# Kernel optimization log

Measured on AMD Instinct MI355X. Metric: run time of the kernel, lower is better.

## Reference

```python
import jax, jax.numpy as jnp
import numpy as np

B, L, D, H, NL, V, W = 4, 2048, 512, 8, 4, 258, 8
HD = D // H


def setup_inputs() -> dict:
    key = jax.random.key(0)
    ks = jax.random.split(key, 12)
    s = 0.02
    x = jax.random.randint(ks[0], (B, L), 0, V, dtype=jnp.int32)
    patch_lengths = jnp.full((B, 256), W, dtype=jnp.int32)  # sum over patches == L
    emb = jax.random.normal(ks[1], (V, D), jnp.float32) * s
    ent_w = jax.random.normal(ks[2], (D, 1), jnp.float32) * s
    ent_b = jnp.zeros((D,), jnp.float32)
    qkv_w = jax.random.normal(ks[3], (NL, 3 * D, D), jnp.float32) * s
    qkv_b = jnp.zeros((NL, 3 * D), jnp.float32)
    ao_w = jax.random.normal(ks[4], (NL, D, D), jnp.float32) * s
    ao_b = jnp.zeros((NL, D), jnp.float32)
    ln1_s = jnp.ones((NL, D), jnp.float32)
    ln1_b = jnp.zeros((NL, D), jnp.float32)
    ln2_s = jnp.ones((NL, D), jnp.float32)
    ln2_b = jnp.zeros((NL, D), jnp.float32)
    ff1_w = jax.random.normal(ks[5], (NL, 4 * D, D), jnp.float32) * s
    ff1_b = jnp.zeros((NL, 4 * D), jnp.float32)
    ff2_w = jax.random.normal(ks[6], (NL, D, 4 * D), jnp.float32) * s
    ff2_b = jnp.zeros((NL, D), jnp.float32)
    out_w = jax.random.normal(ks[7], (V, D), jnp.float32) * s
    return {"emb": emb, "ent_w": ent_w, "ent_b": ent_b, "qkv_w": qkv_w,
            "qkv_b": qkv_b, "ao_w": ao_w, "ao_b": ao_b, "ln1_s": ln1_s,
            "ln1_b": ln1_b, "ln2_s": ln2_s, "ln2_b": ln2_b, "ff1_w": ff1_w,
            "ff1_b": ff1_b, "ff2_w": ff2_w, "ff2_b": ff2_b, "out_w": out_w,
            "x": x, "patch_lengths": patch_lengths}


def _layernorm(h, scale, bias, eps=1e-5):
    mu = jnp.mean(h, axis=-1, keepdims=True)
    var = jnp.mean(jnp.square(h - mu), axis=-1, keepdims=True)
    return (h - mu) * jax.lax.rsqrt(var + eps) * scale + bias


def _entropy_features(x, dtype):
    # fused sliding-window histogram via one-hot cumsum (replaces per-window bincount loop)
    onehot = jax.nn.one_hot(x, 256, dtype=dtype)            # [B, L, 256]
    c = jnp.cumsum(onehot, axis=1)
    cpad = jnp.concatenate([jnp.zeros_like(c[:, :1]), c], axis=1)
    counts = cpad[:, W:] - cpad[:, :-W]                     # [B, L-W+1, 256]
    p = counts / W
    ent = -jnp.sum(p * jnp.log2(p + 1e-10), axis=-1)        # zero-count terms contribute exactly 0
    full = jnp.zeros(x.shape, dtype).at[:, :x.shape[1] - W + 1].set(ent)
    return full[..., None]                                  # [B, L, 1]


def _block(h, p):
    qkv_w, qkv_b, ao_w, ao_b, l1s, l1b, l2s, l2b, f1w, f1b, f2w, f2b = p
    g = _layernorm(h, l1s, l1b)
    qkv = g @ qkv_w.T + qkv_b                                # [B, L, 3D]
    q, k, v = jnp.split(qkv, 3, axis=-1)
    q = q.reshape(B, L, H, HD)
    k = k.reshape(B, L, H, HD)
    v = v.reshape(B, L, H, HD)
    scores = jnp.einsum('blhd,bmhd->bhlm', q, k) / np.sqrt(HD).astype(h.dtype)
    attn = jax.nn.softmax(scores, axis=-1)
    o = jnp.einsum('bhlm,bmhd->blhd', attn, v).reshape(B, L, D)
    h = h + o @ ao_w.T + ao_b
    g = _layernorm(h, l2s, l2b)
    g = jax.nn.gelu(g @ f1w.T + f1b, approximate=False) @ f2w.T + f2b
    return h + g, None


def reference(emb, ent_w, ent_b, qkv_w, qkv_b, ao_w, ao_b, ln1_s, ln1_b,
              ln2_s, ln2_b, ff1_w, ff1_b, ff2_w, ff2_b, out_w, x, patch_lengths):
    tok = emb[x]                                             # [B, L, D]
    ent = _entropy_features(x, tok.dtype)                    # [B, L, 1]
    ent_emb = ent * ent_w[:, 0] + ent_b                      # Linear(1, D)
    h = tok + ent_emb
    h, _ = jax.lax.scan(_block, h,
                        (qkv_w, qkv_b, ao_w, ao_b, ln1_s, ln1_b,
                         ln2_s, ln2_b, ff1_w, ff1_b, ff2_w, ff2_b))
    # NOTE: the original module's global_transformer/patch-pool branch does not
    # feed the returned logits (dead code); logits come from the local stream h.
    logits = h @ out_w.T                                     # [B, L, V]
    return logits
```

## Files before the change

kernel.cpp:

```cpp
#include <hip/hip_runtime.h>
#include <hip/hip_bf16.h>
#include <math.h>

#define BB 4
#define LL 2048
#define DD 512
#define HH 8
#define NLAYER 4
#define VV 258
#define WW 8
#define HDIM 64
#define MM (BB * LL)
#define VPAD 384

typedef __attribute__((ext_vector_type(8))) short short8v;
typedef __attribute__((ext_vector_type(4))) float float4v;

typedef __attribute__((address_space(3))) unsigned int lds_u32;
typedef const __attribute__((address_space(1))) unsigned int glb_u32;

__device__ __forceinline__ unsigned short f2bf(float x) {
    unsigned int u = __float_as_uint(x);
    unsigned int r = (u + 0x7fffu + ((u >> 16) & 1u)) >> 16;
    return (unsigned short)r;
}

__device__ __forceinline__ unsigned lds_addr(const void* p) {
    return (unsigned)(size_t)(__attribute__((address_space(3))) const void*)p;
}

__global__ __launch_bounds__(256)
void cvt_kernel(const float* __restrict__ in, unsigned short* __restrict__ out, int n)
{
    int i = (blockIdx.x * 256 + threadIdx.x) * 4;
    if (i < n) {
        float4 v = *reinterpret_cast<const float4*>(in + i);
        uint2 pk;
        pk.x = (unsigned)f2bf(v.x) | ((unsigned)f2bf(v.y) << 16);
        pk.y = (unsigned)f2bf(v.z) | ((unsigned)f2bf(v.w) << 16);
        *reinterpret_cast<uint2*>(out + i) = pk;
    }
}

__global__ __launch_bounds__(256)
void cvt_pad_kernel(const float* __restrict__ in, unsigned short* __restrict__ out)
{
    int i = blockIdx.x * 256 + threadIdx.x;
    int row = i >> 9;
    out[i] = (row < VV) ? f2bf(in[i]) : (unsigned short)0;
}

__global__ __launch_bounds__(256)
void embed_ln_kernel(const int* __restrict__ x,
                     const float* __restrict__ emb,
                     const float* __restrict__ ent_w,
                     const float* __restrict__ ent_b,
                     const float* __restrict__ ln_s,
                     const float* __restrict__ ln_b,
                     float* __restrict__ h,
                     unsigned short* __restrict__ g)
{
    int w = threadIdx.x >> 6, lane = threadIdx.x & 63;
    int row = blockIdx.x * 4 + w;
    int b = row / LL, l = row % LL;

    float ent = 0.f;
    if (l <= LL - WW) {
        int win[WW];
        #pragma unroll
        for (int i = 0; i < WW; i++) win[i] = x[b * LL + l + i];
        float s = 0.f;
        #pragma unroll
        for (int i = 0; i < WW; i++) {
            if (win[i] < 256) {
                int c = 0;
                #pragma unroll
                for (int j = 0; j < WW; j++) c += (win[j] == win[i]) ? 1 : 0;
                s += log2f((float)c * 0.125f + 1e-10f);
            }
        }
        ent = -s * 0.125f;
    }

    int tok = x[row];
    const float* erow = emb + (size_t)tok * DD + lane * 8;
    float v[8], ew[8], eb[8];
    *reinterpret_cast<float4*>(v)      = *reinterpret_cast<const float4*>(erow);
    *reinterpret_cast<float4*>(v + 4)  = *reinterpret_cast<const float4*>(erow + 4);
    *reinterpret_cast<float4*>(ew)     = *reinterpret_cast<const float4*>(ent_w + lane * 8);
    *reinterpret_cast<float4*>(ew + 4) = *reinterpret_cast<const float4*>(ent_w + lane * 8 + 4);
    *reinterpret_cast<float4*>(eb)     = *reinterpret_cast<const float4*>(ent_b + lane * 8);
    *reinterpret_cast<float4*>(eb + 4) = *reinterpret_cast<const float4*>(ent_b + lane * 8 + 4);

    float sum = 0.f, sq = 0.f;
    #pragma unroll
    for (int i = 0; i < 8; i++) {
        v[i] = v[i] + ent * ew[i] + eb[i];
        sum += v[i]; sq += v[i] * v[i];
    }
    float* hr = h + (size_t)row * DD + lane * 8;
    *reinterpret_cast<float4*>(hr)     = *reinterpret_cast<const float4*>(v);
    *reinterpret_cast<float4*>(hr + 4) = *reinterpret_cast<const float4*>(v + 4);

    #pragma unroll
    for (int off = 32; off > 0; off >>= 1) {
        sum += __shfl_xor(sum, off);
        sq  += __shfl_xor(sq, off);
    }
    float mu = sum * (1.f / DD);
    float var = sq * (1.f / DD) - mu * mu;
    float rstd = rsqrtf(var + 1e-5f);

    float s8[8], bi[8];
    *reinterpret_cast<float4*>(s8)     = *reinterpret_cast<const float4*>(ln_s + lane * 8);
    *reinterpret_cast<float4*>(s8 + 4) = *reinterpret_cast<const float4*>(ln_s + lane * 8 + 4);
    *reinterpret_cast<float4*>(bi)     = *reinterpret_cast<const float4*>(ln_b + lane * 8);
    *reinterpret_cast<float4*>(bi + 4) = *reinterpret_cast<const float4*>(ln_b + lane * 8 + 4);

    unsigned int pk[4];
    #pragma unroll
    for (int i = 0; i < 4; i++) {
        unsigned short lo = f2bf((v[2*i]   - mu) * rstd * s8[2*i]   + bi[2*i]);
        unsigned short hi = f2bf((v[2*i+1] - mu) * rstd * s8[2*i+1] + bi[2*i+1]);
        pk[i] = (unsigned)lo | ((unsigned)hi << 16);
    }
    *reinterpret_cast<uint4*>(g + (size_t)row * DD + lane * 8) =
        *reinterpret_cast<const uint4*>(pk);
}

__global__ __launch_bounds__(256)
void ln_kernel(const float* __restrict__ h,
               const float* __restrict__ scale,
               const float* __restrict__ bias,
               unsigned short* __restrict__ g)
{
    int w = threadIdx.x >> 6, lane = threadIdx.x & 63;
    int row = blockIdx.x * 4 + w;
    const float* hr = h + (size_t)row * DD + lane * 8;

    float v[8];
    *reinterpret_cast<float4*>(v)     = *reinterpret_cast<const float4*>(hr);
    *reinterpret_cast<float4*>(v + 4) = *reinterpret_cast<const float4*>(hr + 4);

    float sum = 0.f, sq = 0.f;
    #pragma unroll
    for (int i = 0; i < 8; i++) { sum += v[i]; sq += v[i] * v[i]; }
    #pragma unroll
    for (int off = 32; off > 0; off >>= 1) {
        sum += __shfl_xor(sum, off);
        sq  += __shfl_xor(sq, off);
    }
    float mu = sum * (1.f / DD);
    float var = sq * (1.f / DD) - mu * mu;
    float rstd = rsqrtf(var + 1e-5f);

    float s[8], bi[8];
    *reinterpret_cast<float4*>(s)      = *reinterpret_cast<const float4*>(scale + lane * 8);
    *reinterpret_cast<float4*>(s + 4)  = *reinterpret_cast<const float4*>(scale + lane * 8 + 4);
    *reinterpret_cast<float4*>(bi)     = *reinterpret_cast<const float4*>(bias + lane * 8);
    *reinterpret_cast<float4*>(bi + 4) = *reinterpret_cast<const float4*>(bias + lane * 8 + 4);

    unsigned int pk[4];
    #pragma unroll
    for (int i = 0; i < 4; i++) {
        unsigned short lo = f2bf((v[2*i]   - mu) * rstd * s[2*i]   + bi[2*i]);
        unsigned short hi = f2bf((v[2*i+1] - mu) * rstd * s[2*i+1] + bi[2*i+1]);
        pk[i] = (unsigned)lo | ((unsigned)hi << 16);
    }
    *reinterpret_cast<uint4*>(g + (size_t)row * DD + lane * 8) =
        *reinterpret_cast<const uint4*>(pk);
}

template<bool HAS_BIAS, bool GELU, bool RESID, int OMODE>
__global__ __launch_bounds__(256)
void gemm_mfma(const unsigned short* __restrict__ A,
               const unsigned short* __restrict__ W,
               const float* __restrict__ bias,
               const float* __restrict__ resid,
               void* __restrict__ Cv,
               unsigned short* __restrict__ Cb,
               int Nn, int Kk)
{
    __shared__ unsigned short As[2][128 * 64];
    __shared__ unsigned short Bs[2][128 * 64];

    int t = threadIdx.x;
    int w = t >> 6, lane = t & 63;
    int wr = w >> 1, wc = w & 1;
    int l15 = lane & 15, l4 = lane >> 4;
    int m0 = blockIdx.y * 128, n0 = blockIdx.x * 128;

    int lrow = lane >> 3;
    int segp = (lane & 7) ^ lrow;

    float4v acc[4][4];
    #pragma unroll
    for (int i = 0; i < 4; i++)
        #pragma unroll
        for (int j = 0; j < 4; j++)
            acc[i][j] = (float4v){0.f, 0.f, 0.f, 0.f};

    #define STAGE(buf, k0) do {                                                   \
        _Pragma("unroll")                                                         \
        for (int i_ = 0; i_ < 4; i_++) {                                          \
            int r_ = i_ * 32 + w * 8 + lrow;                                      \
            __builtin_amdgcn_global_load_lds(                                     \
                (glb_u32*)(A + (size_t)(m0 + r_) * Kk + (k0) + segp * 8),         \
                (lds_u32*)(As[buf] + i_ * 2048 + w * 512), 16, 0, 0);             \
            __builtin_amdgcn_global_load_lds(                                     \
                (glb_u32*)(W + (size_t)(n0 + r_) * Kk + (k0) + segp * 8),         \
                (lds_u32*)(Bs[buf] + i_ * 2048 + w * 512), 16, 0, 0);             \
        } } while (0)

    int nk = Kk >> 6;
    STAGE(0, 0);
    for (int kt = 0; kt < nk; kt++) {
        int cur = kt & 1;
        if (kt + 1 < nk) {
            STAGE(cur ^ 1, (kt + 1) << 6);
            __builtin_amdgcn_sched_barrier(0);
            asm volatile("s_waitcnt vmcnt(8)");
            __builtin_amdgcn_sched_barrier(0);
        } else {
            __builtin_amdgcn_sched_barrier(0);
            asm volatile("s_waitcnt vmcnt(0)");
            __builtin_amdgcn_sched_barrier(0);
        }
        __builtin_amdgcn_s_barrier();

        const char* asb = (const char*)As[cur];
        const char* bsb = (const char*)Bs[cur];
        #pragma unroll
        for (int kc = 0; kc < 2; kc++) {
            short8v af[4], bfr[4];
            #pragma unroll
            for (int mf = 0; mf < 4; mf++) {
                int row = wr * 64 + mf * 16 + l15;
                int off = (row * 128 + kc * 64 + l4 * 16) ^ ((row & 7) << 4);
                af[mf] = *reinterpret_cast<const short8v*>(asb + off);
            }
            #pragma unroll
            for (int nf = 0; nf < 4; nf++) {
                int row = wc * 64 + nf * 16 + l15;
                int off = (row * 128 + kc * 64 + l4 * 16) ^ ((row & 7) << 4);
                bfr[nf] = *reinterpret_cast<const short8v*>(bsb + off);
            }
            #pragma unroll
            for (int mf = 0; mf < 4; mf++)
                #pragma unroll
                for (int nf = 0; nf < 4; nf++)
                    acc[mf][nf] = __builtin_amdgcn_mfma_f32_16x16x32_bf16(
                        af[mf], bfr[nf], acc[mf][nf], 0, 0, 0);
        }
        __builtin_amdgcn_s_barrier();
    }
    #undef STAGE

    #pragma unroll
    for (int mf = 0; mf < 4; mf++)
        #pragma unroll
        for (int nf = 0; nf < 4; nf++)
            #pragma unroll
            for (int r = 0; r < 4; r++) {
                int m = m0 + wr * 64 + mf * 16 + l4 * 4 + r;
                int n = n0 + wc * 64 + nf * 16 + l15;
                if (n < Nn) {
                    float v = acc[mf][nf][r];
                    if (HAS_BIAS) v += bias[n];
                    if (GELU)     v = 0.5f * v * (1.f + erff(v * 0.70710678118654752f));
                    if (RESID)    v += resid[(size_t)m * Nn + n];
                    if (OMODE == 1) {
                        ((unsigned short*)Cv)[(size_t)m * Nn + n] = f2bf(v);
                    } else {
                        ((float*)Cv)[(size_t)m * Nn + n] = v;
                        if (OMODE == 2) Cb[(size_t)m * Nn + n] = f2bf(v);
                    }
                }
            }
}

__global__ __launch_bounds__(512, 2)
void attn_mfma(const unsigned short* __restrict__ qkv, unsigned short* __restrict__ o)
{
    __shared__ unsigned short Kl[2][64 * 64];
    __shared__ unsigned short Vs[2][64 * 64];
    __shared__ unsigned short Pl[8 * 16 * 64];
    __shared__ float Scl[8][16];

    int t = threadIdx.x, w = t >> 6, lane = t & 63;
    int l15 = lane & 15, l4 = lane >> 4;

    int flat = blockIdx.x;
    int swz = (flat & 7) * 64 + (flat >> 3);
    int qt = swz & 15, hh = (swz >> 4) & 7, b = swz >> 7;

    int q0 = qt * 128 + w * 16;
    const int RS = 3 * DD;

    short8v qf[2];
    #pragma unroll
    for (int dh = 0; dh < 2; dh++) {
        size_t addr = (size_t)(b * LL + q0 + l15) * RS + hh * HDIM + dh * 32 + l4 * 8;
        qf[dh] = *reinterpret_cast<const short8v*>(qkv + addr);
    }

    float4v o_acc[4];
    #pragma unroll
    for (int dt = 0; dt < 4; dt++) o_acc[dt] = (float4v){0.f, 0.f, 0.f, 0.f};
    float m_run = -1e30f, l_run = 0.f;

    char* pbase = (char*)Pl + w * 2048;

    int krow = t >> 3, kseg = t & 7;
    int vrow = ((t >> 5) << 2) | ((t >> 1) & 3);
    int vseg = (((t >> 3) & 3) << 1) | (t & 1);
    int koff = (krow * 128 + kseg * 16) ^ ((krow & 7) << 4);
    int voff = t * 16;

    const unsigned short* kptr = qkv + (size_t)(b * LL + krow) * RS + hh * HDIM + DD + kseg * 8;
    const unsigned short* vptr = qkv + (size_t)(b * LL + vrow) * RS + hh * HDIM + 2 * DD + vseg * 8;
    const int step = 64 * RS;

    unsigned vtrbase = lds_addr(Vs) + ((lane >> 4) << 10)
                     + (((lane >> 2) & 3) << 5) + ((lane & 3) << 3);

    {
        short8v krg = *reinterpret_cast<const short8v*>(kptr); kptr += step;
        short8v vrg = *reinterpret_cast<const short8v*>(vptr); vptr += step;
        *reinterpret_cast<short8v*>((char*)Kl[0] + koff) = krg;
        *reinterpret_cast<short8v*>((char*)Vs[0] + voff) = vrg;
    }
    __syncthreads();

    for (int kb = 0; kb < LL / 64; kb++) {
        int cur = kb & 1;
        short8v krg, vrg;
        if (kb + 1 < LL / 64) {
            krg = *reinterpret_cast<const short8v*>(kptr); kptr += step;
            vrg = *reinterpret_cast<const short8v*>(vptr); vptr += step;
        }

        const char* klc = (const char*)Kl[cur];
        unsigned vb = vtrbase + cur * 8192;

        float4v s_acc[4];
        __builtin_amdgcn_s_setprio(1);
        #pragma unroll
        for (int nt = 0; nt < 4; nt++) {
            s_acc[nt] = (float4v){0.f, 0.f, 0.f, 0.f};
            #pragma unroll
            for (int dh = 0; dh < 2; dh++) {
                int row = nt * 16 + l15;
                int off = (row * 128 + dh * 64 + l4 * 16) ^ ((row & 7) << 4);
                short8v kf = *reinterpret_cast<const short8v*>(klc + off);
                s_acc[nt] = __builtin_amdgcn_mfma_f32_16x16x32_bf16(kf, qf[dh], s_acc[nt], 0, 0, 0);
            }
        }
        __builtin_amdgcn_s_setprio(0);

        float mm = -1e30f;
        #pragma unroll
        for (int nt = 0; nt < 4; nt++)
            #pragma unroll
            for (int r = 0; r < 4; r++)
                mm = fmaxf(mm, s_acc[nt][r]);
        mm *= 0.125f;
        mm = fmaxf(mm, __shfl_xor(mm, 16));
        mm = fmaxf(mm, __shfl_xor(mm, 32));

        if (!__all(mm <= m_run + 8.f)) {
            float mnew = fmaxf(m_run, mm);
            float sc = __expf(m_run - mnew);
            m_run = mnew;
            l_run *= sc;
            if (l4 == 0) Scl[w][l15] = sc;
            float4 scv = *reinterpret_cast<const float4*>(&Scl[w][l4 * 4]);
            #pragma unroll
            for (int dt = 0; dt < 4; dt++) {
                o_acc[dt][0] *= scv.x; o_acc[dt][1] *= scv.y;
                o_acc[dt][2] *= scv.z; o_acc[dt][3] *= scv.w;
            }
        }

        float ps = 0.f;
        #pragma unroll
        for (int nt = 0; nt < 4; nt++) {
            float p0 = __expf(fmaf(s_acc[nt][0], 0.125f, -m_run));
            float p1 = __expf(fmaf(s_acc[nt][1], 0.125f, -m_run));
            float p2 = __expf(fmaf(s_acc[nt][2], 0.125f, -m_run));
            float p3 = __expf(fmaf(s_acc[nt][3], 0.125f, -m_run));
            ps += (p0 + p1) + (p2 + p3);
            unsigned int pk0, pk1;
            asm("v_cvt_pk_bf16_f32 %0, %1, %2" : "=v"(pk0) : "v"(p0), "v"(p1));
            asm("v_cvt_pk_bf16_f32 %0, %1, %2" : "=v"(pk1) : "v"(p2), "v"(p3));
            uint2 pk; pk.x = pk0; pk.y = pk1;
            int off = (l15 * 128 + nt * 32 + l4 * 8) ^ ((l15 & 7) << 4);
            *reinterpret_cast<uint2*>(pbase + off) = pk;
        }
        l_run += ps;

        #pragma unroll
        for (int kc = 0; kc < 2; kc++) {
            int poff = (l15 * 128 + kc * 64 + l4 * 16) ^ ((l15 & 7) << 4);
            short8v pf = *reinterpret_cast<const short8v*>(pbase + poff);
            unsigned long long tr0, tr1, tr2, tr3, tr4, tr5, tr6, tr7;
            unsigned ab = vb + kc * 4096;
            asm volatile("ds_read_b64_tr_b16 %0, %1" : "=v"(tr0) : "v"(ab));
            asm volatile("ds_read_b64_tr_b16 %0, %1" : "=v"(tr1) : "v"(ab + 512));
            asm volatile("ds_read_b64_tr_b16 %0, %1" : "=v"(tr2) : "v"(ab + 128));
            asm volatile("ds_read_b64_tr_b16 %0, %1" : "=v"(tr3) : "v"(ab + 640));
            asm volatile("ds_read_b64_tr_b16 %0, %1" : "=v"(tr4) : "v"(ab + 256));
            asm volatile("ds_read_b64_tr_b16 %0, %1" : "=v"(tr5) : "v"(ab + 768));
            asm volatile("ds_read_b64_tr_b16 %0, %1" : "=v"(tr6) : "v"(ab + 384));
            asm volatile("ds_read_b64_tr_b16 %0, %1" : "=v"(tr7) : "v"(ab + 896));
            asm volatile("s_waitcnt lgkmcnt(0)");
            __builtin_amdgcn_sched_barrier(0);
            __builtin_amdgcn_s_setprio(1);
            union { unsigned long long q[2]; short8v v; } u0, u1, u2, u3;
            u0.q[0] = tr0; u0.q[1] = tr1;
            u1.q[0] = tr2; u1.q[1] = tr3;
            u2.q[0] = tr4; u2.q[1] = tr5;
            u3.q[0] = tr6; u3.q[1] = tr7;
            o_acc[0] = __builtin_amdgcn_mfma_f32_16x16x32_bf16(pf, u0.v, o_acc[0], 0, 0, 0);
            o_acc[1] = __builtin_amdgcn_mfma_f32_16x16x32_bf16(pf, u1.v, o_acc[1], 0, 0, 0);
            o_acc[2] = __builtin_amdgcn_mfma_f32_16x16x32_bf16(pf, u2.v, o_acc[2], 0, 0, 0);
            o_acc[3] = __builtin_amdgcn_mfma_f32_16x16x32_bf16(pf, u3.v, o_acc[3], 0, 0, 0);
            __builtin_amdgcn_s_setprio(0);
        }

        if (kb + 1 < LL / 64) {
            *reinterpret_cast<short8v*>((char*)Kl[cur ^ 1] + koff) = krg;
            *reinterpret_cast<short8v*>((char*)Vs[cur ^ 1] + voff) = vrg;
        }
        __syncthreads();
    }

    float lt = l_run;
    lt += __shfl_xor(lt, 16);
    lt += __shfl_xor(lt, 32);
    if (l4 == 0) Scl[w][l15] = 1.f / lt;
    float4 iv = *reinterpret_cast<const float4*>(&Scl[w][l4 * 4]);
    float invs[4] = {iv.x, iv.y, iv.z, iv.w};
    #pragma unroll
    for (int r = 0; r < 4; r++) {
        int qg = q0 + l4 * 4 + r;
        #pragma unroll
        for (int dt = 0; dt < 4; dt++) {
            o[(size_t)(b * LL + qg) * DD + hh * HDIM + dt * 16 + l15] =
                f2bf(o_acc[dt][r] * invs[r]);
        }
    }
}

extern "C" void kernel_launch(void* const* d_in, const int* in_sizes, int n_in,
                              void* d_out, int out_size, void* d_ws, size_t ws_size,
                              hipStream_t stream)
{
    const float* emb    = (const float*)d_in[0];
    const float* ent_w  = (const float*)d_in[1];
    const float* ent_b  = (const float*)d_in[2];
    const float* qkv_w  = (const float*)d_in[3];
    const float* qkv_b  = (const float*)d_in[4];
    const float* ao_w   = (const float*)d_in[5];
    const float* ao_b   = (const float*)d_in[6];
    const float* ln1_s  = (const float*)d_in[7];
    const float* ln1_b  = (const float*)d_in[8];
    const float* ln2_s  = (const float*)d_in[9];
    const float* ln2_b  = (const float*)d_in[10];
    const float* ff1_w  = (const float*)d_in[11];
    const float* ff1_b  = (const float*)d_in[12];
    const float* ff2_w  = (const float*)d_in[13];
    const float* ff2_b  = (const float*)d_in[14];
    const float* out_w  = (const float*)d_in[15];
    const int*   x      = (const int*)d_in[16];

    float* out = (float*)d_out;

    const int NQW = NLAYER * 3 * DD * DD;
    const int NAW = NLAYER * DD * DD;
    const int NF1 = NLAYER * 4 * DD * DD;
    const int NF2 = NLAYER * DD * 4 * DD;

    char* p = (char*)d_ws;
    unsigned short* wq  = (unsigned short*)p; p += (size_t)NQW * 2;
    unsigned short* wa  = (unsigned short*)p; p += (size_t)NAW * 2;
    unsigned short* w1  = (unsigned short*)p; p += (size_t)NF1 * 2;
    unsigned short* w2  = (unsigned short*)p; p += (size_t)NF2 * 2;
    unsigned short* wob = (unsigned short*)p; p += (size_t)VPAD * DD * 2;
    float*          h   = (float*)p;          p += (size_t)MM * DD * 4;
    unsigned short* hb  = (unsigned short*)p; p += (size_t)MM * DD * 2;
    unsigned short* gb  = (unsigned short*)p; p += (size_t)MM * DD * 2;
    unsigned short* ob  = (unsigned short*)p; p += (size_t)MM * DD * 2;
    unsigned short* bb  = (unsigned short*)p; p += (size_t)MM * 4 * DD * 2;

    dim3 blk(256);

    cvt_kernel<<<NQW / 1024, blk, 0, stream>>>(qkv_w, wq, NQW);
    cvt_kernel<<<NAW / 1024, blk, 0, stream>>>(ao_w,  wa, NAW);
    cvt_kernel<<<NF1 / 1024, blk, 0, stream>>>(ff1_w, w1, NF1);
    cvt_kernel<<<NF2 / 1024, blk, 0, stream>>>(ff2_w, w2, NF2);
    cvt_pad_kernel<<<(VPAD * DD) / 256, blk, 0, stream>>>(out_w, wob);

    embed_ln_kernel<<<MM / 4, blk, 0, stream>>>(x, emb, ent_w, ent_b,
                                                ln1_s, ln1_b, h, gb);

    for (int layer = 0; layer < NLAYER; layer++) {
        const unsigned short* qw = wq + (size_t)layer * 3 * DD * DD;
        const unsigned short* aw = wa + (size_t)layer * DD * DD;
        const unsigned short* f1 = w1 + (size_t)layer * 4 * DD * DD;
        const unsigned short* f2 = w2 + (size_t)layer * DD * 4 * DD;
        const float* qb  = qkv_b + (size_t)layer * 3 * DD;
        const float* ab  = ao_b  + (size_t)layer * DD;
        const float* l1s = ln1_s + (size_t)layer * DD;
        const float* l1b = ln1_b + (size_t)layer * DD;
        const float* l2s = ln2_s + (size_t)layer * DD;
        const float* l2b = ln2_b + (size_t)layer * DD;
        const float* f1b = ff1_b + (size_t)layer * 4 * DD;
        const float* f2b = ff2_b + (size_t)layer * DD;

        if (layer > 0)
            ln_kernel<<<MM / 4, blk, 0, stream>>>(h, l1s, l1b, gb);

        {
            dim3 grid((3 * DD) / 128, MM / 128);
            gemm_mfma<true, false, false, 1><<<grid, blk, 0, stream>>>(
                gb, qw, qb, nullptr, bb, nullptr, 3 * DD, DD);
        }

        attn_mfma<<<512, 512, 0, stream>>>(bb, ob);

        {
            dim3 grid(DD / 128, MM / 128);
            gemm_mfma<true, false, true, 0><<<grid, blk, 0, stream>>>(
                ob, aw, ab, h, h, nullptr, DD, DD);
        }

        ln_kernel<<<MM / 4, blk, 0, stream>>>(h, l2s, l2b, gb);

        {
            dim3 grid((4 * DD) / 128, MM / 128);
            gemm_mfma<true, true, false, 1><<<grid, blk, 0, stream>>>(
                gb, f1, f1b, nullptr, bb, nullptr, 4 * DD, DD);
        }

        {
            dim3 grid(DD / 128, MM / 128);
            if (layer == NLAYER - 1)
                gemm_mfma<true, false, true, 2><<<grid, blk, 0, stream>>>(
                    bb, f2, f2b, h, h, hb, DD, 4 * DD);
            else
                gemm_mfma<true, false, true, 0><<<grid, blk, 0, stream>>>(
                    bb, f2, f2b, h, h, nullptr, DD, 4 * DD);
        }
    }

    {
        dim3 grid(VPAD / 128, MM / 128);
        gemm_mfma<false, false, false, 0><<<grid, blk, 0, stream>>>(
            hb, wob, nullptr, nullptr, out, nullptr, VV, DD);
    }
}
```

Measured before the change: 782.2 us.

## Narrow GEMM N-tile for small-N GEMMs and restructure attention softmax/PV loads

Templates the GEMM on the N-tile width and uses 64-wide tiles for the N=512 and vocab GEMMs, doubling the block count so more CUs are occupied. In attention, switches the softmax to exp2 with the scale pre-multiplied by log2(e), and issues all P and V transposed LDS reads up front with staged waitcnts so MFMAs start while later reads are still in flight. The narrower tiles give less B-tile reuse per loaded A tile, and the hand-written waitcnt sequencing depends on the reads completing in issue order.

Result: no change. 788.1 us (+0.8%).

```diff
diff --git a/kernel.cpp b/kernel.cpp
--- a/kernel.cpp
+++ b/kernel.cpp
@@ -13,6 +13,9 @@
 #define MM (BB * LL)
 #define VPAD 384
 
+#define C8 0.18033688f
+#define THR2 11.54156f
+
 typedef __attribute__((ext_vector_type(8))) short short8v;
 typedef __attribute__((ext_vector_type(4))) float float4v;
 
@@ -171,7 +174,7 @@
         *reinterpret_cast<const uint4*>(pk);
 }
 
-template<bool HAS_BIAS, bool GELU, bool RESID, int OMODE>
+template<bool HAS_BIAS, bool GELU, bool RESID, int OMODE, int BN>
 __global__ __launch_bounds__(256)
 void gemm_mfma(const unsigned short* __restrict__ A,
                const unsigned short* __restrict__ W,
@@ -181,23 +184,24 @@
                unsigned short* __restrict__ Cb,
                int Nn, int Kk)
 {
+    constexpr int NF = BN / 32;
     __shared__ unsigned short As[2][128 * 64];
-    __shared__ unsigned short Bs[2][128 * 64];
+    __shared__ unsigned short Bs[2][BN * 64];
 
     int t = threadIdx.x;
     int w = t >> 6, lane = t & 63;
     int wr = w >> 1, wc = w & 1;
     int l15 = lane & 15, l4 = lane >> 4;
-    int m0 = blockIdx.y * 128, n0 = blockIdx.x * 128;
+    int m0 = blockIdx.y * 128, n0 = blockIdx.x * BN;
 
     int lrow = lane >> 3;
     int segp = (lane & 7) ^ lrow;
 
-    float4v acc[4][4];
+    float4v acc[4][NF];
     #pragma unroll
     for (int i = 0; i < 4; i++)
         #pragma unroll
-        for (int j = 0; j < 4; j++)
+        for (int j = 0; j < NF; j++)
             acc[i][j] = (float4v){0.f, 0.f, 0.f, 0.f};
 
     #define STAGE(buf, k0) do {                                                   \
@@ -207,6 +211,10 @@
             __builtin_amdgcn_global_load_lds(                                     \
                 (glb_u32*)(A + (size_t)(m0 + r_) * Kk + (k0) + segp * 8),         \
                 (lds_u32*)(As[buf] + i_ * 2048 + w * 512), 16, 0, 0);             \
+        }                                                                         \
+        _Pragma("unroll")                                                         \
+        for (int i_ = 0; i_ < NF; i_++) {                                         \
+            int r_ = i_ * 32 + w * 8 + lrow;                                      \
             __builtin_amdgcn_global_load_lds(                                     \
                 (glb_u32*)(W + (size_t)(n0 + r_) * Kk + (k0) + segp * 8),         \
                 (lds_u32*)(Bs[buf] + i_ * 2048 + w * 512), 16, 0, 0);             \
@@ -219,7 +227,8 @@
         if (kt + 1 < nk) {
             STAGE(cur ^ 1, (kt + 1) << 6);
             __builtin_amdgcn_sched_barrier(0);
-            asm volatile("s_waitcnt vmcnt(8)");
+            if constexpr (BN == 128) asm volatile("s_waitcnt vmcnt(8)");
+            else                     asm volatile("s_waitcnt vmcnt(6)");
             __builtin_amdgcn_sched_barrier(0);
         } else {
             __builtin_amdgcn_sched_barrier(0);
@@ -232,7 +241,7 @@
         const char* bsb = (const char*)Bs[cur];
         #pragma unroll
         for (int kc = 0; kc < 2; kc++) {
-            short8v af[4], bfr[4];
+            short8v af[4], bfr[NF];
             #pragma unroll
             for (int mf = 0; mf < 4; mf++) {
                 int row = wr * 64 + mf * 16 + l15;
@@ -240,15 +249,15 @@
                 af[mf] = *reinterpret_cast<const short8v*>(asb + off);
             }
             #pragma unroll
-            for (int nf = 0; nf < 4; nf++) {
-                int row = wc * 64 + nf * 16 + l15;
+            for (int nf = 0; nf < NF; nf++) {
+                int row = wc * (BN / 2) + nf * 16 + l15;
                 int off = (row * 128 + kc * 64 + l4 * 16) ^ ((row & 7) << 4);
                 bfr[nf] = *reinterpret_cast<const short8v*>(bsb + off);
             }
             #pragma unroll
             for (int mf = 0; mf < 4; mf++)
                 #pragma unroll
-                for (int nf = 0; nf < 4; nf++)
+                for (int nf = 0; nf < NF; nf++)
                     acc[mf][nf] = __builtin_amdgcn_mfma_f32_16x16x32_bf16(
                         af[mf], bfr[nf], acc[mf][nf], 0, 0, 0);
         }
@@ -259,11 +268,11 @@
     #pragma unroll
     for (int mf = 0; mf < 4; mf++)
         #pragma unroll
-        for (int nf = 0; nf < 4; nf++)
+        for (int nf = 0; nf < NF; nf++)
             #pragma unroll
             for (int r = 0; r < 4; r++) {
                 int m = m0 + wr * 64 + mf * 16 + l4 * 4 + r;
-                int n = n0 + wc * 64 + nf * 16 + l15;
+                int n = n0 + wc * (BN / 2) + nf * 16 + l15;
                 if (n < Nn) {
                     float v = acc[mf][nf][r];
                     if (HAS_BIAS) v += bias[n];
@@ -323,6 +332,9 @@
 
     unsigned vtrbase = lds_addr(Vs) + ((lane >> 4) << 10)
                      + (((lane >> 2) & 3) << 5) + ((lane & 3) << 3);
+    unsigned pswz = (unsigned)((l15 & 7) << 4);
+    unsigned pa0 = lds_addr(pbase) + ((unsigned)(l15 * 128 + l4 * 16) ^ pswz);
+    unsigned pa1 = lds_addr(pbase) + ((unsigned)(l15 * 128 + 64 + l4 * 16) ^ pswz);
 
     {
         short8v krg = *reinterpret_cast<const short8v*>(kptr); kptr += step;
@@ -358,19 +370,20 @@
         }
         __builtin_amdgcn_s_setprio(0);
 
-        float mm = -1e30f;
-        #pragma unroll
-        for (int nt = 0; nt < 4; nt++)
-            #pragma unroll
-            for (int r = 0; r < 4; r++)
-                mm = fmaxf(mm, s_acc[nt][r]);
-        mm *= 0.125f;
+        float t0 = fmaxf(fmaxf(s_acc[0][0], s_acc[0][1]), s_acc[0][2]);
+        float t1 = fmaxf(fmaxf(s_acc[0][3], s_acc[1][0]), s_acc[1][1]);
+        float t2 = fmaxf(fmaxf(s_acc[1][2], s_acc[1][3]), s_acc[2][0]);
+        float t3 = fmaxf(fmaxf(s_acc[2][1], s_acc[2][2]), s_acc[2][3]);
+        float t4 = fmaxf(fmaxf(s_acc[3][0], s_acc[3][1]), s_acc[3][2]);
+        float mm = fmaxf(fmaxf(fmaxf(t0, t1), t2),
+                         fmaxf(fmaxf(t3, t4), s_acc[3][3]));
+        mm *= C8;
         mm = fmaxf(mm, __shfl_xor(mm, 16));
         mm = fmaxf(mm, __shfl_xor(mm, 32));
 
-        if (!__all(mm <= m_run + 8.f)) {
+        if (!__all(mm <= m_run + THR2)) {
             float mnew = fmaxf(m_run, mm);
-            float sc = __expf(m_run - mnew);
+            float sc = __builtin_amdgcn_exp2f(m_run - mnew);
             m_run = mnew;
             l_run *= sc;
             if (l4 == 0) Scl[w][l15] = sc;
@@ -385,10 +398,10 @@
         float ps = 0.f;
         #pragma unroll
         for (int nt = 0; nt < 4; nt++) {
-            float p0 = __expf(fmaf(s_acc[nt][0], 0.125f, -m_run));
-            float p1 = __expf(fmaf(s_acc[nt][1], 0.125f, -m_run));
-            float p2 = __expf(fmaf(s_acc[nt][2], 0.125f, -m_run));
-            float p3 = __expf(fmaf(s_acc[nt][3], 0.125f, -m_run));
+            float p0 = __builtin_amdgcn_exp2f(fmaf(s_acc[nt][0], C8, -m_run));
+            float p1 = __builtin_amdgcn_exp2f(fmaf(s_acc[nt][1], C8, -m_run));
+            float p2 = __builtin_amdgcn_exp2f(fmaf(s_acc[nt][2], C8, -m_run));
+            float p3 = __builtin_amdgcn_exp2f(fmaf(s_acc[nt][3], C8, -m_run));
             ps += (p0 + p1) + (p2 + p3);
             unsigned int pk0, pk1;
             asm("v_cvt_pk_bf16_f32 %0, %1, %2" : "=v"(pk0) : "v"(p0), "v"(p1));
@@ -399,34 +412,55 @@
         }
         l_run += ps;
 
-        #pragma unroll
-        for (int kc = 0; kc < 2; kc++) {
-            int poff = (l15 * 128 + kc * 64 + l4 * 16) ^ ((l15 & 7) << 4);
-            short8v pf = *reinterpret_cast<const short8v*>(pbase + poff);
-            unsigned long long tr0, tr1, tr2, tr3, tr4, tr5, tr6, tr7;
-            unsigned ab = vb + kc * 4096;
-            asm volatile("ds_read_b64_tr_b16 %0, %1" : "=v"(tr0) : "v"(ab));
-            asm volatile("ds_read_b64_tr_b16 %0, %1" : "=v"(tr1) : "v"(ab + 512));
-            asm volatile("ds_read_b64_tr_b16 %0, %1" : "=v"(tr2) : "v"(ab + 128));
-            asm volatile("ds_read_b64_tr_b16 %0, %1" : "=v"(tr3) : "v"(ab + 640));
-            asm volatile("ds_read_b64_tr_b16 %0, %1" : "=v"(tr4) : "v"(ab + 256));
-            asm volatile("ds_read_b64_tr_b16 %0, %1" : "=v"(tr5) : "v"(ab + 768));
-            asm volatile("ds_read_b64_tr_b16 %0, %1" : "=v"(tr6) : "v"(ab + 384));
-            asm volatile("ds_read_b64_tr_b16 %0, %1" : "=v"(tr7) : "v"(ab + 896));
-            asm volatile("s_waitcnt lgkmcnt(0)");
-            __builtin_amdgcn_sched_barrier(0);
-            __builtin_amdgcn_s_setprio(1);
-            union { unsigned long long q[2]; short8v v; } u0, u1, u2, u3;
-            u0.q[0] = tr0; u0.q[1] = tr1;
-            u1.q[0] = tr2; u1.q[1] = tr3;
-            u2.q[0] = tr4; u2.q[1] = tr5;
-            u3.q[0] = tr6; u3.q[1] = tr7;
-            o_acc[0] = __builtin_amdgcn_mfma_f32_16x16x32_bf16(pf, u0.v, o_acc[0], 0, 0, 0);
-            o_acc[1] = __builtin_amdgcn_mfma_f32_16x16x32_bf16(pf, u1.v, o_acc[1], 0, 0, 0);
-            o_acc[2] = __builtin_amdgcn_mfma_f32_16x16x32_bf16(pf, u2.v, o_acc[2], 0, 0, 0);
-            o_acc[3] = __builtin_amdgcn_mfma_f32_16x16x32_bf16(pf, u3.v, o_acc[3], 0, 0, 0);
-            __builtin_amdgcn_s_setprio(0);
-        }
+        short8v pf0, pf1;
+        asm volatile("ds_read_b128 %0, %1" : "=v"(pf0) : "v"(pa0) : "memory");
+        asm volatile("ds_read_b128 %0, %1" : "=v"(pf1) : "v"(pa1) : "memory");
+        unsigned long long a0, a1, a2, a3, a4, a5, a6, a7;
+        unsigned long long b0, b1, b2, b3, b4, b5, b6, b7;
+        unsigned ab0 = vb, ab1 = vb + 4096;
+        asm volatile("ds_read_b64_tr_b16 %0, %1" : "=v"(a0) : "v"(ab0));
+        asm volatile("ds_read_b64_tr_b16 %0, %1" : "=v"(a1) : "v"(ab0 + 512));
+        asm volatile("ds_read_b64_tr_b16 %0, %1" : "=v"(a2) : "v"(ab0 + 128));
+        asm volatile("ds_read_b64_tr_b16 %0, %1" : "=v"(a3) : "v"(ab0 + 640));
+        asm volatile("ds_read_b64_tr_b16 %0, %1" : "=v"(a4) : "v"(ab0 + 256));
+        asm volatile("ds_read_b64_tr_b16 %0, %1" : "=v"(a5) : "v"(ab0 + 768));
+        asm volatile("ds_read_b64_tr_b16 %0, %1" : "=v"(a6) : "v"(ab0 + 384));
+        asm volatile("ds_read_b64_tr_b16 %0, %1" : "=v"(a7) : "v"(ab0 + 896));
+        asm volatile("ds_read_b64_tr_b16 %0, %1" : "=v"(b0) : "v"(ab1));
+        asm volatile("ds_read_b64_tr_b16 %0, %1" : "=v"(b1) : "v"(ab1 + 512));
+        asm volatile("ds_read_b64_tr_b16 %0, %1" : "=v"(b2) : "v"(ab1 + 128));
+        asm volatile("ds_read_b64_tr_b16 %0, %1" : "=v"(b3) : "v"(ab1 + 640));
+        asm volatile("ds_read_b64_tr_b16 %0, %1" : "=v"(b4) : "v"(ab1 + 256));
+        asm volatile("ds_read_b64_tr_b16 %0, %1" : "=v"(b5) : "v"(ab1 + 768));
+        asm volatile("ds_read_b64_tr_b16 %0, %1" : "=v"(b6) : "v"(ab1 + 384));
+        asm volatile("ds_read_b64_tr_b16 %0, %1" : "=v"(b7) : "v"(ab1 + 896));
+        union { unsigned long long q[2]; short8v v; } u0, u1, u2, u3;
+        __builtin_amdgcn_s_setprio(1);
+        asm volatile("s_waitcnt lgkmcnt(12)");
+        __builtin_amdgcn_sched_barrier(0);
+        u0.q[0] = a0; u0.q[1] = a1;
+        u1.q[0] = a2; u1.q[1] = a3;
+        o_acc[0] = __builtin_amdgcn_mfma_f32_16x16x32_bf16(pf0, u0.v, o_acc[0], 0, 0, 0);
+        o_acc[1] = __builtin_amdgcn_mfma_f32_16x16x32_bf16(pf0, u1.v, o_acc[1], 0, 0, 0);
+        asm volatile("s_waitcnt lgkmcnt(8)");
+        __builtin_amdgcn_sched_barrier(0);
+        u2.q[0] = a4; u2.q[1] = a5;
+        u3.q[0] = a6; u3.q[1] = a7;
+        o_acc[2] = __builtin_amdgcn_mfma_f32_16x16x32_bf16(pf0, u2.v, o_acc[2], 0, 0, 0);
+        o_acc[3] = __builtin_amdgcn_mfma_f32_16x16x32_bf16(pf0, u3.v, o_acc[3], 0, 0, 0);
+        asm volatile("s_waitcnt lgkmcnt(4)");
+        __builtin_amdgcn_sched_barrier(0);
+        u0.q[0] = b0; u0.q[1] = b1;
+        u1.q[0] = b2; u1.q[1] = b3;
+        o_acc[0] = __builtin_amdgcn_mfma_f32_16x16x32_bf16(pf1, u0.v, o_acc[0], 0, 0, 0);
+        o_acc[1] = __builtin_amdgcn_mfma_f32_16x16x32_bf16(pf1, u1.v, o_acc[1], 0, 0, 0);
+        asm volatile("s_waitcnt lgkmcnt(0)");
+        __builtin_amdgcn_sched_barrier(0);
+        u2.q[0] = b4; u2.q[1] = b5;
+        u3.q[0] = b6; u3.q[1] = b7;
+        o_acc[2] = __builtin_amdgcn_mfma_f32_16x16x32_bf16(pf1, u2.v, o_acc[2], 0, 0, 0);
+        o_acc[3] = __builtin_amdgcn_mfma_f32_16x16x32_bf16(pf1, u3.v, o_acc[3], 0, 0, 0);
+        __builtin_amdgcn_s_setprio(0);
 
         if (kb + 1 < LL / 64) {
             *reinterpret_cast<short8v*>((char*)Kl[cur ^ 1] + koff) = krg;
@@ -523,15 +557,15 @@
 
         {
             dim3 grid((3 * DD) / 128, MM / 128);
-            gemm_mfma<true, false, false, 1><<<grid, blk, 0, stream>>>(
+            gemm_mfma<true, false, false, 1, 128><<<grid, blk, 0, stream>>>(
                 gb, qw, qb, nullptr, bb, nullptr, 3 * DD, DD);
         }
 
         attn_mfma<<<512, 512, 0, stream>>>(bb, ob);
 
         {
-            dim3 grid(DD / 128, MM / 128);
-            gemm_mfma<true, false, true, 0><<<grid, blk, 0, stream>>>(
+            dim3 grid(DD / 64, MM / 128);
+            gemm_mfma<true, false, true, 0, 64><<<grid, blk, 0, stream>>>(
                 ob, aw, ab, h, h, nullptr, DD, DD);
         }
 
@@ -539,24 +573,24 @@
 
         {
             dim3 grid((4 * DD) / 128, MM / 128);
-            gemm_mfma<true, true, false, 1><<<grid, blk, 0, stream>>>(
+            gemm_mfma<true, true, false, 1, 128><<<grid, blk, 0, stream>>>(
                 gb, f1, f1b, nullptr, bb, nullptr, 4 * DD, DD);
         }
 
         {
-            dim3 grid(DD / 128, MM / 128);
+            dim3 grid(DD / 64, MM / 128);
             if (layer == NLAYER - 1)
-                gemm_mfma<true, false, true, 2><<<grid, blk, 0, stream>>>(
+                gemm_mfma<true, false, true, 2, 64><<<grid, blk, 0, stream>>>(
                     bb, f2, f2b, h, h, hb, DD, 4 * DD);
             else
-                gemm_mfma<true, false, true, 0><<<grid, blk, 0, stream>>>(
+                gemm_mfma<true, false, true, 0, 64><<<grid, blk, 0, stream>>>(
                     bb, f2, f2b, h, h, nullptr, DD, 4 * DD);
         }
     }
 
     {
-        dim3 grid(VPAD / 128, MM / 128);
-        gemm_mfma<false, false, false, 0><<<grid, blk, 0, stream>>>(
+        dim3 grid(VPAD / 64, MM / 128);
+        gemm_mfma<false, false, false, 0, 64><<<grid, blk, 0, stream>>>(
             hb, wob, nullptr, nullptr, out, nullptr, VV, DD);
     }
 }
```
